# Kernel optimization log

Measured on AMD Instinct MI355X. Metric: run time of the kernel, lower is better.

## Reference

```python
import jax, jax.numpy as jnp
import numpy as np

D_MODEL = 2048
B, L = 4, 2048


def _dwconv(x, w, b):
    # x: (B, D, L), w: (D, 1, 3), b: (D,). Causal depthwise conv (PyTorch pad=2 then [...,:L]).
    y = jax.lax.conv_general_dilated(
        x, w, window_strides=(1,), padding=[(2, 0)],
        feature_group_count=x.shape[1], dimension_numbers=("NCH", "OIH", "NCH"))
    return y + b[None, :, None]


def setup_inputs() -> dict:
    key = jax.random.key(0)
    ks = jax.random.split(key, 12)
    D = D_MODEL
    s = 0.02
    inp = {
        "u": jax.random.normal(ks[0], (B, L, D), jnp.float32),
        "Wq": jax.random.normal(ks[1], (D, D), jnp.float32) * s,
        "bq": jnp.zeros((D,), jnp.float32),
        "Wk": jax.random.normal(ks[2], (D, D), jnp.float32) * s,
        "bk": jnp.zeros((D,), jnp.float32),
        "Wv": jax.random.normal(ks[3], (D, D), jnp.float32) * s,
        "bv": jnp.zeros((D,), jnp.float32),
        "convq_w": jax.random.normal(ks[4], (D, 1, 3), jnp.float32) * 0.5,
        "convq_b": jnp.zeros((D,), jnp.float32),
        "convk_w": jax.random.normal(ks[5], (D, 1, 3), jnp.float32) * 0.5,
        "convk_b": jnp.zeros((D,), jnp.float32),
        "ssm_kernel": jax.random.normal(ks[6], (D, L), jnp.float32) * 0.01,  # H = d_model (head_dim=1)
        "D_skip": jax.random.normal(ks[7], (D,), jnp.float32),
        "Wo": jax.random.normal(ks[8], (D, D), jnp.float32) * s,
        "bo": jnp.zeros((D,), jnp.float32),
    }
    return inp


def reference(u, Wq, bq, Wk, bk, Wv, bv, convq_w, convq_b, convk_w, convk_b,
              ssm_kernel, D_skip, Wo, bo):
    # u: (B, L, H)  head_dim = 1 so H == d_model
    Lq = u.shape[1]
    fft_size = 2 * Lq  # L_kernel + L with l_max=None, rate=1

    # q/k/v projections (W @ u.T + b in torch == u @ W.T + b)
    q = jnp.einsum("blh,eh->ble", u, Wq) + bq
    k = jnp.einsum("blh,eh->ble", u, Wk) + bk
    v = jnp.einsum("blh,eh->ble", u, Wv) + bv
    q = jnp.transpose(q, (0, 2, 1))  # (B, H, L)
    k = jnp.transpose(k, (0, 2, 1))
    v = jnp.transpose(v, (0, 2, 1))

    # causal depthwise short convs
    q = _dwconv(q, convq_w, convq_b)
    k = _dwconv(k, convk_w, convk_b)

    # head_dim = 1: kv outer product collapses to elementwise product (B, H, L)
    kv = k * v

    # FFT long convolution: torch does rfft(kv)/n * rfft(kernel), irfft norm='forward'
    # which equals the standard unnormalized circular conv below.
    kv_f = jnp.fft.rfft(kv, n=fft_size)
    kernel_f = jnp.fft.rfft(ssm_kernel, n=fft_size)  # (H, F)
    y = jnp.fft.irfft(kv_f * kernel_f, n=fft_size)[..., :Lq]

    # D skip and q gating
    y = (y + kv * D_skip[None, :, None]) * q  # (B, H, L)

    # output projection
    y = jnp.transpose(y, (0, 2, 1))  # (B, L, H)
    return jnp.einsum("blh,eh->ble", y, Wo) + bo
```

## Files before the change

kernel.cpp:

```cpp
#include <hip/hip_runtime.h>
#include <cstdint>
#include <cstddef>

#define DD 2048
#define LL 2048
#define BB 4
#define MM (BB * LL)
#define NN 6144

typedef __bf16 bf16;
typedef __bf16 bf16x8 __attribute__((ext_vector_type(8)));
typedef __bf16 bf16x4 __attribute__((ext_vector_type(4)));
typedef __bf16 bf16x2 __attribute__((ext_vector_type(2)));
typedef float f32x4 __attribute__((ext_vector_type(4)));

__device__ __forceinline__ void gload16(const void* g, void* l) {
    __builtin_amdgcn_global_load_lds(
        (const __attribute__((address_space(1))) void*)g,
        (__attribute__((address_space(3))) void*)l, 16, 0, 0);
}

__global__ __launch_bounds__(256) void cvt_all(
    const float* __restrict__ u, const float* __restrict__ wq,
    const float* __restrict__ wk, const float* __restrict__ wv,
    const float* __restrict__ wo, bf16* __restrict__ u_bf,
    bf16* __restrict__ wqkv, bf16* __restrict__ wo_bf) {
    const int blk = blockIdx.x;
    const float* s;
    bf16* d;
    int base;
    if (blk < 8192)       { s = u;  d = u_bf;            base = 0; }
    else if (blk < 10240) { s = wq; d = wqkv;            base = 8192; }
    else if (blk < 12288) { s = wk; d = wqkv + 4194304;  base = 10240; }
    else if (blk < 14336) { s = wv; d = wqkv + 8388608;  base = 12288; }
    else                  { s = wo; d = wo_bf;           base = 14336; }
    const int i = (blk - base) * 256 + threadIdx.x;
    const float4* sp = (const float4*)s + (size_t)i * 2;
    float4 a = sp[0], b = sp[1];
    bf16x8 o;
    o[0] = (bf16)a.x; o[1] = (bf16)a.y; o[2] = (bf16)a.z; o[3] = (bf16)a.w;
    o[4] = (bf16)b.x; o[5] = (bf16)b.y; o[6] = (bf16)b.z; o[7] = (bf16)b.w;
    *((bf16x8*)d + i) = o;
}

__device__ __forceinline__ void stage_half(const bf16* g, bf16* l, size_t rstep, int tid) {
    gload16(g, l + tid * 8);
    gload16(g + rstep, l + 4096 + tid * 8);
}

#define MFMA_BLK(AF, BQ, IOFF)                                                  \
    __builtin_amdgcn_s_setprio(1);                                              \
    _Pragma("unroll") for (int j = 0; j < 4; j++)                               \
        _Pragma("unroll") for (int i = 0; i < 4; i++)                           \
            acc[(IOFF) + i][j] = __builtin_amdgcn_mfma_f32_16x16x32_bf16(       \
                AF[i], BQ[j], acc[(IOFF) + i][j], 0, 0, 0);                     \
    __builtin_amdgcn_s_setprio(0);

template <int NT>
__device__ __forceinline__ void mma256_loop(const bf16* gA, const bf16* gB,
                                            int Kdim, bf16* lds,
                                            f32x4 (&acc)[8][4]) {
    const int tid = threadIdx.x;
    const int wave = tid >> 6, lane = tid & 63;
    const int wm = wave >> 2, wn = wave & 3;
    const int fm = lane & 15, fg = lane >> 4;
    const size_t rstep = (size_t)128 * Kdim;
    const int koff = ((fg ^ ((fm >> 1) & 3)) << 3);
    const int aoff = (wm * 128 + fm) * 32 + koff;
    const int boff = (wn * 64 + fm) * 32 + koff;

    bf16* const A0 = lds;
    bf16* const B0 = lds + 32768;

#pragma unroll
    for (int i = 0; i < 8; i++)
#pragma unroll
        for (int j = 0; j < 4; j++) acc[i][j] = (f32x4){0.f, 0.f, 0.f, 0.f};

    stage_half(gA, A0, rstep, tid);
    stage_half(gB, B0, rstep, tid);
    stage_half(gA + 32, A0 + 8192, rstep, tid);
    stage_half(gB + 32, B0 + 8192, rstep, tid);

    bf16x8 af0[4], af1[4], bq0[4], bq1[4];

    for (int t = 0; t < NT; ++t) {
        const int c = t & 1;
        bf16* const Ac = A0 + c * 16384;
        bf16* const Bc = B0 + c * 16384;
        bf16* const An = A0 + (c ^ 1) * 16384;
        bf16* const Bn = B0 + (c ^ 1) * 16384;
        const bf16* a1 = gA + (t + 1) * 64;
        const bf16* b1 = gB + (t + 1) * 64;
        const bool st = (t + 1 < NT);

        asm volatile("s_waitcnt vmcnt(4)" ::: "memory");
        asm volatile("s_barrier" ::: "memory");
#pragma unroll
        for (int i = 0; i < 4; i++) af0[i] = *(const bf16x8*)(Ac + aoff + i * 512);
#pragma unroll
        for (int j = 0; j < 4; j++) bq0[j] = *(const bf16x8*)(Bc + boff + j * 512);
        if (st) stage_half(a1, An, rstep, tid);
#pragma unroll
        for (int i = 0; i < 4; i++) af1[i] = *(const bf16x8*)(Ac + aoff + (i + 4) * 512);
        MFMA_BLK(af0, bq0, 0)
        if (st) stage_half(b1, Bn, rstep, tid);

        if (st) { asm volatile("s_waitcnt vmcnt(4)" ::: "memory"); }
        else    { asm volatile("s_waitcnt vmcnt(0)" ::: "memory"); }
        asm volatile("s_barrier" ::: "memory");
#pragma unroll
        for (int i = 0; i < 4; i++) af0[i] = *(const bf16x8*)(Ac + 8192 + aoff + i * 512);
#pragma unroll
        for (int j = 0; j < 4; j++) bq1[j] = *(const bf16x8*)(Bc + 8192 + boff + j * 512);
        if (st) stage_half(a1 + 32, An + 8192, rstep, tid);
        MFMA_BLK(af1, bq0, 4)
#pragma unroll
        for (int i = 0; i < 4; i++) af1[i] = *(const bf16x8*)(Ac + 8192 + aoff + (i + 4) * 512);
        if (st) stage_half(b1 + 32, Bn + 8192, rstep, tid);
        MFMA_BLK(af0, bq1, 0)
        MFMA_BLK(af1, bq1, 4)
    }
}

__global__ __launch_bounds__(512, 2) void gemm_qkv(const bf16* __restrict__ A,
                                                   const bf16* __restrict__ Bm,
                                                   const float* __restrict__ bqp,
                                                   const float* __restrict__ bkp,
                                                   const float* __restrict__ bvp,
                                                   bf16* __restrict__ CtOut) {
    __shared__ bf16 lds[65536];
    const int id = blockIdx.x;
    const int xcd = id & 7, li = id >> 3;
    const int m0 = (xcd * 4 + (li & 3)) << 8;
    const int n0 = (li >> 2) << 8;

    const int tid = threadIdx.x;
    const int wave = tid >> 6, lane = tid & 63;
    const int srow = tid >> 2;
    const int skx = (((lane & 3) ^ ((lane >> 3) & 3)) << 3);
    const bf16* gA = A + (size_t)(m0 + srow) * DD + skx;
    const bf16* gB = Bm + (size_t)(n0 + srow) * DD + skx;

    f32x4 acc[8][4];
    mma256_loop<DD / 64>(gA, gB, DD, lds, acc);

    __syncthreads();
    const int wm = wave >> 2, wn = wave & 3;
    const int fm = lane & 15, fg = lane >> 4;
    const float* bp = (n0 < 2048) ? bqp : ((n0 < 4096) ? bkp : bvp);
    const int nb = n0 & 2047;
#pragma unroll
    for (int j = 0; j < 4; j++) {
        const int col = wn * 64 + j * 16 + fm;
        const float bvv = bp[nb + col];
        const int csw = (col & 7) << 3;
#pragma unroll
        for (int i = 0; i < 8; i++) {
            const int row = (wm * 128 + i * 16 + fg * 4) ^ csw;
            bf16x4 o;
#pragma unroll
            for (int r = 0; r < 4; r++) o[r] = (bf16)(acc[i][j][r] + bvv);
            *(bf16x4*)&lds[col * 256 + row] = o;
        }
    }
    __syncthreads();
    const int ccol = tid >> 5, chunk = tid & 31;
#pragma unroll
    for (int p = 0; p < 16; p++) {
        const int col = p * 16 + ccol;
        bf16x8 vv = *(const bf16x8*)&lds[col * 256 + ((chunk * 8) ^ ((col & 7) << 3))];
        *(bf16x8*)(CtOut + (size_t)(n0 + col) * MM + m0 + chunk * 8) = vv;
    }
}

__global__ __launch_bounds__(512, 2) void gemm_bt_f32(const bf16* __restrict__ A,
                                                      const bf16* __restrict__ Bm,
                                                      const float* __restrict__ bias,
                                                      float* __restrict__ C,
                                                      int Ndim, int Kdim) {
    __shared__ bf16 lds[65536];
    const int id = blockIdx.x;
    const int xcd = id & 7, li = id >> 3;
    const int m0 = (xcd * 4 + (li & 3)) << 8;
    const int n0 = (li >> 2) << 8;

    const int tid = threadIdx.x;
    const int wave = tid >> 6, lane = tid & 63;
    const int srow = tid >> 2;
    const int skx = (((lane & 3) ^ ((lane >> 3) & 3)) << 3);
    const bf16* gA = A + (size_t)(m0 + srow) * Kdim + skx;
    const bf16* gB = Bm + (size_t)(n0 + srow) * Kdim + skx;

    f32x4 acc[8][4];
    mma256_loop<DD / 64>(gA, gB, Kdim, lds, acc);

    const int wm = wave >> 2, wn = wave & 3;
    const int fm = lane & 15, fg = lane >> 4;
#pragma unroll
    for (int j = 0; j < 4; j++) {
        const int col = n0 + wn * 64 + j * 16 + fm;
        const float bvv = bias[col];
#pragma unroll
        for (int i = 0; i < 8; i++) {
#pragma unroll
            for (int r = 0; r < 4; r++) {
                const int row = m0 + wm * 128 + i * 16 + fg * 4 + r;
                C[(size_t)row * Ndim + col] = acc[i][j][r] + bvv;
            }
        }
    }
}

__global__ __launch_bounds__(256) void dwconv_kv2(
    const bf16* __restrict__ qkvT,
    const float* __restrict__ cqw, const float* __restrict__ cqb,
    const float* __restrict__ ckw, const float* __restrict__ ckb,
    bf16* __restrict__ qcT, bf16* __restrict__ kvT) {
    const int bid = blockIdx.x;
    const int b = bid >> 11, d = bid & (DD - 1);
    const int tid = threadIdx.x;
    const int l = tid * 8;

    const bf16* qR = qkvT + (size_t)d * MM + b * LL;
    const bf16* kR = qkvT + (size_t)(2048 + d) * MM + b * LL;
    const bf16* vR = qkvT + (size_t)(4096 + d) * MM + b * LL;

    const float q0 = cqw[d * 3], q1 = cqw[d * 3 + 1], q2 = cqw[d * 3 + 2];
    const float k0 = ckw[d * 3], k1 = ckw[d * 3 + 1], k2 = ckw[d * 3 + 2];
    const float qb = cqb[d], kb = ckb[d];

    bf16x8 qx = *(const bf16x8*)(qR + l);
    bf16x8 kx = *(const bf16x8*)(kR + l);
    bf16x8 vx = *(const bf16x8*)(vR + l);

    float xq[10], xk[10];
    xq[0] = 0.f; xq[1] = 0.f; xk[0] = 0.f; xk[1] = 0.f;
    if (l >= 2) {
        bf16x2 qh = *(const bf16x2*)(qR + l - 2);
        bf16x2 kh = *(const bf16x2*)(kR + l - 2);
        xq[0] = (float)qh[0]; xq[1] = (float)qh[1];
        xk[0] = (float)kh[0]; xk[1] = (float)kh[1];
    }
#pragma unroll
    for (int c = 0; c < 8; c++) { xq[c + 2] = (float)qx[c]; xk[c + 2] = (float)kx[c]; }

    bf16x8 oq, okv;
#pragma unroll
    for (int c = 0; c < 8; c++) {
        float qc = q0 * xq[c] + q1 * xq[c + 1] + q2 * xq[c + 2] + qb;
        float kc = k0 * xk[c] + k1 * xk[c + 1] + k2 * xk[c + 2] + kb;
        oq[c] = (bf16)qc;
        okv[c] = (bf16)(kc * (float)vx[c]);
    }
    const size_t o = ((size_t)b * DD + d) * LL + l;
    *(bf16x8*)(qcT + o) = oq;
    *(bf16x8*)(kvT + o) = okv;
}

#define KVS 2120
__global__ __launch_bounds__(128, 2) void longconv_gate(
    const bf16* __restrict__ kvT, const bf16* __restrict__ qcT,
    const float* __restrict__ kern, const float* __restrict__ Dskip,
    bf16* __restrict__ ygT) {
    __shared__ bf16 kv_ls[4 * KVS];
    __shared__ float krev_f[2112];
    const int d = blockIdx.x;
    const int tid = threadIdx.x;

    {
        const int bb = tid >> 5, t32 = tid & 31;
#pragma unroll
        for (int c = 0; c < 8; ++c) {
            const int l = (c * 32 + t32) * 8;
            bf16x8 v = *(const bf16x8*)(kvT + ((size_t)bb * DD + d) * LL + l);
            *(bf16x8*)&kv_ls[KVS * bb + 48 + l] = v;
        }
        if (tid < 48) {
#pragma unroll
            for (int b2 = 0; b2 < 4; b2++) kv_ls[KVS * b2 + tid] = (bf16)0.f;
        } else if (tid < 64) {
#pragma unroll
            for (int b2 = 0; b2 < 4; b2++) kv_ls[KVS * b2 + 2048 + tid] = (bf16)0.f;
        } else if (tid < 72) {
#pragma unroll
            for (int b2 = 0; b2 < 4; b2++) kv_ls[KVS * b2 + 2048 + tid] = (bf16)0.f;
        }
    }
    {
        const float* kr = kern + (size_t)d * LL;
#pragma unroll
        for (int c = 0; c < 16; ++c) {
            const int x = c * 128 + tid;
            krev_f[x] = kr[2047 - x];
        }
        if (tid < 64) krev_f[2048 + tid] = 0.f;
    }
    __syncthreads();

    const int lane = tid & 63;
    const int w = __builtin_amdgcn_readfirstlane(tid >> 6);
    const int n = lane & 15, q = lane >> 4;
    const int b = n & 3, pp = n >> 2;
    const int cB = KVS * b + 16 * pp + 8 * q;

    f32x4 acc[16];
#pragma unroll
    for (int s = 0; s < 16; s++) acc[s] = (f32x4){0.f, 0.f, 0.f, 0.f};

    for (int it = 0; it < 64; ++it) {
        const int as = 2031 - 32 * it - n + 8 * q;
        float af[8];
#pragma unroll
        for (int j = 0; j < 8; j++) af[j] = krev_f[as + j];
        bf16x8 a;
#pragma unroll
        for (int j = 0; j < 8; j++) a[j] = (bf16)af[j];

        const int bbase = cB + 64 * w + 32 - 32 * it;
#pragma unroll
        for (int h = 0; h < 2; ++h) {
            bf16x8 bfr[8];
#pragma unroll
            for (int s8 = 0; s8 < 8; s8++) {
                const int s = h * 8 + s8;
                if (it <= 4 * s + 2 * w + 1)
                    bfr[s8] = *(const bf16x8*)&kv_ls[bbase + 128 * s];
            }
#pragma unroll
            for (int s8 = 0; s8 < 8; s8++) {
                const int s = h * 8 + s8;
                if (it <= 4 * s + 2 * w + 1)
                    acc[s] = __builtin_amdgcn_mfma_f32_16x16x32_bf16(
                        a, bfr[s8], acc[s], 0, 0, 0);
            }
        }
    }

    const float dsk = Dskip[d];
#pragma unroll
    for (int s = 0; s < 16; s++) {
        const int i = 2 * s + w;
        const int l = 64 * i + 16 * pp + 4 * q;
        const size_t gb = ((size_t)b * DD + d) * LL + l;
        bf16x4 qc4 = *(const bf16x4*)&qcT[gb];
        bf16x4 kv4 = *(const bf16x4*)&kv_ls[KVS * b + 48 + l];
        bf16x4 o;
#pragma unroll
        for (int r = 0; r < 4; r++) {
            float val = (acc[s][r] + (float)kv4[r] * dsk) * (float)qc4[r];
            o[r] = (bf16)val;
        }
        *(bf16x4*)&ygT[gb] = o;
    }
}

__global__ __launch_bounds__(256) void transpose_dl(const bf16* __restrict__ src,
                                                    bf16* __restrict__ dst) {
    __shared__ bf16 ts[64 * 64];
    const int b = blockIdx.z;
    const int l0 = blockIdx.x * 64, d0 = blockIdx.y * 64;
    const int tid = threadIdx.x;
    {
        const int r0 = tid >> 3, c8 = tid & 7;
#pragma unroll
        for (int h = 0; h < 2; h++) {
            const int r = r0 + h * 32;
            bf16x8 v = *(const bf16x8*)&src[((size_t)b * DD + d0 + r) * LL + l0 + c8 * 8];
            *(bf16x8*)&ts[r * 64 + ((c8 ^ (r & 7)) << 3)] = v;
        }
    }
    __syncthreads();
    const int l = tid & 63, dc0 = (tid >> 6) << 3;
#pragma unroll
    for (int half = 0; half < 2; half++) {
        const int dc = dc0 + half * 32;
        bf16x8 o;
#pragma unroll
        for (int j = 0; j < 8; j++) {
            const int r = dc + j;
            o[j] = ts[r * 64 + (((l >> 3) ^ (r & 7)) << 3) + (l & 7)];
        }
        *(bf16x8*)&dst[((size_t)b * LL + l0 + l) * DD + d0 + dc] = o;
    }
}

extern "C" void kernel_launch(void* const* d_in, const int* in_sizes, int n_in,
                              void* d_out, int out_size, void* d_ws, size_t ws_size,
                              hipStream_t stream) {
    const float* u   = (const float*)d_in[0];
    const float* Wq  = (const float*)d_in[1];
    const float* bq  = (const float*)d_in[2];
    const float* Wk  = (const float*)d_in[3];
    const float* bk  = (const float*)d_in[4];
    const float* Wv  = (const float*)d_in[5];
    const float* bv  = (const float*)d_in[6];
    const float* cqw = (const float*)d_in[7];
    const float* cqb = (const float*)d_in[8];
    const float* ckw = (const float*)d_in[9];
    const float* ckb = (const float*)d_in[10];
    const float* ssm = (const float*)d_in[11];
    const float* Dsk = (const float*)d_in[12];
    const float* Wo  = (const float*)d_in[13];
    const float* bo  = (const float*)d_in[14];

    char* w = (char*)d_ws;
    bf16* u_bf    = (bf16*)(w);
    bf16* Wqkv_bf = (bf16*)(w + 33554432ull);
    bf16* Wo_bf   = (bf16*)(w + 58720256ull);
    bf16* qkvT    = (bf16*)(w + 67108864ull);
    bf16* qcT     = (bf16*)(w + 167772160ull);
    bf16* kvT     = (bf16*)(w + 201326592ull);

    cvt_all<<<16384, 256, 0, stream>>>(u, Wq, Wk, Wv, Wo, u_bf, Wqkv_bf, Wo_bf);

    gemm_qkv<<<(MM / 256) * (NN / 256), 512, 0, stream>>>(u_bf, Wqkv_bf, bq, bk, bv, qkvT);

    dwconv_kv2<<<BB * DD, 256, 0, stream>>>(qkvT, cqw, cqb, ckw, ckb, qcT, kvT);

    bf16* ygT = u_bf;
    longconv_gate<<<DD, 128, 0, stream>>>(kvT, qcT, ssm, Dsk, ygT);

    bf16* ygTT = qkvT;
    dim3 gc(LL / 64, DD / 64, BB);
    transpose_dl<<<gc, 256, 0, stream>>>(ygT, ygTT);

    gemm_bt_f32<<<(MM / 256) * (DD / 256), 512, 0, stream>>>(ygTT, Wo_bf, bo,
                                                             (float*)d_out, DD, DD);
}
```

Before: 575.2 us.

## Fuse depthwise conv and k*v product into long-conv gating kernel

The separate depthwise-conv kernel is removed. Each long-conv block now reads q, k and v for its channel straight from the QKV projection output. It computes the causal short convs and k*v in registers and stores kv and qc in LDS, so the qcT and kvT global round trips and one kernel launch go away. In exchange, LDS use per block rises because qc gets its own buffer, and the row stride drops from 2120 to 2112, which may change bank-conflict behaviour. The load phase also runs on fewer, smaller blocks than before.

```diff
diff --git a/kernel.cpp b/kernel.cpp
--- a/kernel.cpp
+++ b/kernel.cpp
@@ -212,81 +212,27 @@
     }
 }
 
-__global__ __launch_bounds__(256) void dwconv_kv2(
+#define KVS 2112
+__global__ __launch_bounds__(128, 2) void dwlc_gate(
     const bf16* __restrict__ qkvT,
     const float* __restrict__ cqw, const float* __restrict__ cqb,
     const float* __restrict__ ckw, const float* __restrict__ ckb,
-    bf16* __restrict__ qcT, bf16* __restrict__ kvT) {
-    const int bid = blockIdx.x;
-    const int b = bid >> 11, d = bid & (DD - 1);
-    const int tid = threadIdx.x;
-    const int l = tid * 8;
-
-    const bf16* qR = qkvT + (size_t)d * MM + b * LL;
-    const bf16* kR = qkvT + (size_t)(2048 + d) * MM + b * LL;
-    const bf16* vR = qkvT + (size_t)(4096 + d) * MM + b * LL;
-
-    const float q0 = cqw[d * 3], q1 = cqw[d * 3 + 1], q2 = cqw[d * 3 + 2];
-    const float k0 = ckw[d * 3], k1 = ckw[d * 3 + 1], k2 = ckw[d * 3 + 2];
-    const float qb = cqb[d], kb = ckb[d];
-
-    bf16x8 qx = *(const bf16x8*)(qR + l);
-    bf16x8 kx = *(const bf16x8*)(kR + l);
-    bf16x8 vx = *(const bf16x8*)(vR + l);
-
-    float xq[10], xk[10];
-    xq[0] = 0.f; xq[1] = 0.f; xk[0] = 0.f; xk[1] = 0.f;
-    if (l >= 2) {
-        bf16x2 qh = *(const bf16x2*)(qR + l - 2);
-        bf16x2 kh = *(const bf16x2*)(kR + l - 2);
-        xq[0] = (float)qh[0]; xq[1] = (float)qh[1];
-        xk[0] = (float)kh[0]; xk[1] = (float)kh[1];
-    }
-#pragma unroll
-    for (int c = 0; c < 8; c++) { xq[c + 2] = (float)qx[c]; xk[c + 2] = (float)kx[c]; }
-
-    bf16x8 oq, okv;
-#pragma unroll
-    for (int c = 0; c < 8; c++) {
-        float qc = q0 * xq[c] + q1 * xq[c + 1] + q2 * xq[c + 2] + qb;
-        float kc = k0 * xk[c] + k1 * xk[c + 1] + k2 * xk[c + 2] + kb;
-        oq[c] = (bf16)qc;
-        okv[c] = (bf16)(kc * (float)vx[c]);
-    }
-    const size_t o = ((size_t)b * DD + d) * LL + l;
-    *(bf16x8*)(qcT + o) = oq;
-    *(bf16x8*)(kvT + o) = okv;
-}
-
-#define KVS 2120
-__global__ __launch_bounds__(128, 2) void longconv_gate(
-    const bf16* __restrict__ kvT, const bf16* __restrict__ qcT,
     const float* __restrict__ kern, const float* __restrict__ Dskip,
     bf16* __restrict__ ygT) {
     __shared__ bf16 kv_ls[4 * KVS];
+    __shared__ bf16 qc_ls[4 * KVS];
     __shared__ float krev_f[2112];
     const int d = blockIdx.x;
     const int tid = threadIdx.x;
 
-    {
-        const int bb = tid >> 5, t32 = tid & 31;
-#pragma unroll
-        for (int c = 0; c < 8; ++c) {
-            const int l = (c * 32 + t32) * 8;
-            bf16x8 v = *(const bf16x8*)(kvT + ((size_t)bb * DD + d) * LL + l);
-            *(bf16x8*)&kv_ls[KVS * bb + 48 + l] = v;
-        }
-        if (tid < 48) {
-#pragma unroll
-            for (int b2 = 0; b2 < 4; b2++) kv_ls[KVS * b2 + tid] = (bf16)0.f;
-        } else if (tid < 64) {
-#pragma unroll
-            for (int b2 = 0; b2 < 4; b2++) kv_ls[KVS * b2 + 2048 + tid] = (bf16)0.f;
-        } else if (tid < 72) {
-#pragma unroll
-            for (int b2 = 0; b2 < 4; b2++) kv_ls[KVS * b2 + 2048 + tid] = (bf16)0.f;
-        }
-    }
+    if (tid < 48) {
+#pragma unroll
+        for (int b2 = 0; b2 < 4; b2++) kv_ls[KVS * b2 + tid] = (bf16)0.f;
+    } else if (tid < 64) {
+#pragma unroll
+        for (int b2 = 0; b2 < 4; b2++) kv_ls[KVS * b2 + 2048 + tid] = (bf16)0.f;
+    }
+
     {
         const float* kr = kern + (size_t)d * LL;
 #pragma unroll
@@ -295,6 +241,48 @@
             krev_f[x] = kr[2047 - x];
         }
         if (tid < 64) krev_f[2048 + tid] = 0.f;
+    }
+
+    {
+        const float q0 = cqw[d * 3], q1 = cqw[d * 3 + 1], q2 = cqw[d * 3 + 2];
+        const float k0 = ckw[d * 3], k1 = ckw[d * 3 + 1], k2 = ckw[d * 3 + 2];
+        const float qb = cqb[d], kb = ckb[d];
+#pragma unroll
+        for (int b = 0; b < 4; ++b) {
+            const bf16* qR = qkvT + (size_t)d * MM + b * LL;
+            const bf16* kR = qkvT + (size_t)(2048 + d) * MM + b * LL;
+            const bf16* vR = qkvT + (size_t)(4096 + d) * MM + b * LL;
+#pragma unroll
+            for (int h = 0; h < 2; ++h) {
+                const int l = tid * 16 + h * 8;
+                bf16x8 qx = *(const bf16x8*)(qR + l);
+                bf16x8 kx = *(const bf16x8*)(kR + l);
+                bf16x8 vx = *(const bf16x8*)(vR + l);
+                float xq[10], xk[10];
+                xq[0] = 0.f; xq[1] = 0.f; xk[0] = 0.f; xk[1] = 0.f;
+                if (l >= 2) {
+                    bf16x2 qh = *(const bf16x2*)(qR + l - 2);
+                    bf16x2 kh = *(const bf16x2*)(kR + l - 2);
+                    xq[0] = (float)qh[0]; xq[1] = (float)qh[1];
+                    xk[0] = (float)kh[0]; xk[1] = (float)kh[1];
+                }
+#pragma unroll
+                for (int c = 0; c < 8; c++) {
+                    xq[c + 2] = (float)qx[c];
+                    xk[c + 2] = (float)kx[c];
+                }
+                bf16x8 oq, okv;
+#pragma unroll
+                for (int c = 0; c < 8; c++) {
+                    float qc = q0 * xq[c] + q1 * xq[c + 1] + q2 * xq[c + 2] + qb;
+                    float kc = k0 * xk[c] + k1 * xk[c + 1] + k2 * xk[c + 2] + kb;
+                    oq[c] = (bf16)qc;
+                    okv[c] = (bf16)(kc * (float)vx[c]);
+                }
+                *(bf16x8*)&kv_ls[KVS * b + 48 + l] = okv;
+                *(bf16x8*)&qc_ls[KVS * b + l] = oq;
+            }
+        }
     }
     __syncthreads();
 
@@ -343,7 +331,7 @@
         const int i = 2 * s + w;
         const int l = 64 * i + 16 * pp + 4 * q;
         const size_t gb = ((size_t)b * DD + d) * LL + l;
-        bf16x4 qc4 = *(const bf16x4*)&qcT[gb];
+        bf16x4 qc4 = *(const bf16x4*)&qc_ls[KVS * b + l];
         bf16x4 kv4 = *(const bf16x4*)&kv_ls[KVS * b + 48 + l];
         bf16x4 o;
 #pragma unroll
@@ -409,17 +397,13 @@
     bf16* Wqkv_bf = (bf16*)(w + 33554432ull);
     bf16* Wo_bf   = (bf16*)(w + 58720256ull);
     bf16* qkvT    = (bf16*)(w + 67108864ull);
-    bf16* qcT     = (bf16*)(w + 167772160ull);
-    bf16* kvT     = (bf16*)(w + 201326592ull);
 
     cvt_all<<<16384, 256, 0, stream>>>(u, Wq, Wk, Wv, Wo, u_bf, Wqkv_bf, Wo_bf);
 
     gemm_qkv<<<(MM / 256) * (NN / 256), 512, 0, stream>>>(u_bf, Wqkv_bf, bq, bk, bv, qkvT);
 
-    dwconv_kv2<<<BB * DD, 256, 0, stream>>>(qkvT, cqw, cqb, ckw, ckb, qcT, kvT);
-
     bf16* ygT = u_bf;
-    longconv_gate<<<DD, 128, 0, stream>>>(kvT, qcT, ssm, Dsk, ygT);
+    dwlc_gate<<<DD, 128, 0, stream>>>(qkvT, cqw, cqb, ckw, ckb, ssm, Dsk, ygT);
 
     bf16* ygTT = qkvT;
     dim3 gc(LL / 64, DD / 64, BB);
```

New measurement: 561.6 us. 1.02x faster.
